# Optimization experiments

Measured on AMD Instinct MI355X. Metric: run time of the kernel, lower is better.

## Reference

```python
import jax, jax.numpy as jnp
import numpy as np
import math

B, S, D, H = 2, 2048, 1024, 16
DH = D // H
PHI = (1 + math.sqrt(5)) / 2

def _carrier_phases(n_heads):
    # DimensionalHeadManager: 7 rungs with weights 1/phi^i, base phases k*pi/7,
    # per-rung heads spread uniformly around the circle.
    base = [k * math.pi / 7 for k in range(7)]
    raw_w = [1.0 / PHI ** i for i in range(7)]
    tw = sum(raw_w)
    alloc = [max(1, round(n_heads * w / tw)) for w in raw_w]
    while sum(alloc) > n_heads:
        alloc[alloc.index(max(alloc))] -= 1
    while sum(alloc) < n_heads:
        alloc[alloc.index(max(alloc))] += 1
    phases = []
    for r, c in enumerate(alloc):
        for j in range(c):
            phases.append(base[r] + 2 * math.pi / max(c, 1) * j)
    return np.array(phases, dtype=np.float32)

def setup_inputs() -> dict:
    key = jax.random.key(0)
    ks = jax.random.split(key, 8)
    x = jax.random.normal(ks[0], (B, S, D), dtype=jnp.float32)
    input_phase = jax.random.uniform(ks[1], (B, S), dtype=jnp.float32) * (2 * math.pi)
    sc = 1.0 / math.sqrt(D)
    Wq = jax.random.normal(ks[2], (D, D), dtype=jnp.float32) * sc
    Wk = jax.random.normal(ks[3], (D, D), dtype=jnp.float32) * sc
    Wv = jax.random.normal(ks[4], (D, D), dtype=jnp.float32) * sc
    Wo = jax.random.normal(ks[5], (D, D), dtype=jnp.float32) * sc
    gamma = jnp.ones((D,), dtype=jnp.float32)
    beta = jnp.zeros((D,), dtype=jnp.float32)
    # per-head fractal compression exponents > 1 (sub-linear for |x|<1)
    exponents = 1.0 + 0.5 * jax.random.uniform(ks[6], (H,), dtype=jnp.float32)
    carrier_phases = jnp.asarray(_carrier_phases(H))
    balance = jnp.asarray(0.5, dtype=jnp.float32)  # BALANCE
    return {"x": x, "input_phase": input_phase, "Wq": Wq, "Wk": Wk, "Wv": Wv,
            "Wo": Wo, "gamma": gamma, "beta": beta, "exponents": exponents,
            "carrier_phases": carrier_phases, "balance": balance}

def _layernorm(x, gamma, beta, eps=1e-5):
    mu = jnp.mean(x, axis=-1, keepdims=True)
    var = jnp.var(x, axis=-1, keepdims=True)
    return (x - mu) * jax.lax.rsqrt(var + eps) * gamma + beta

def _fractal_compress(kv, exps):
    # sign-preserving power-law compression, per-head exponent
    sign = jnp.sign(kv)
    mag = jnp.maximum(jnp.abs(kv), 1e-8)
    return sign * mag ** exps  # exps broadcast (1,H,1,1)

def reference(x, input_phase, Wq, Wk, Wv, Wo, gamma, beta, exponents,
              carrier_phases, balance):
    h = _layernorm(x, gamma, beta)
    def split_heads(t):
        return t.reshape(B, S, H, DH).transpose(0, 2, 1, 3)  # (B,H,S,dh)
    q = split_heads(h @ Wq)
    k = split_heads(h @ Wk)
    v = split_heads(h @ Wv)
    exps = exponents.reshape(1, H, 1, 1)
    k_c = _fractal_compress(k, exps)
    v_c = _fractal_compress(v, exps)
    # per-head carrier resonance: (B,S,H) in [0,1]
    T = jnp.cos((input_phase[:, :, None] - carrier_phases[None, None, :]) / 2.0) ** 2
    Th = T.transpose(0, 2, 1)  # (B,H,S)
    # balance temperature tau = clip(1/(2*balance), 0.1, 10)
    tau = jnp.clip(1.0 / (2.0 * balance + 1e-8), 0.1, 10.0)
    scores = jnp.einsum('bhqd,bhkd->bhqk', q, k_c) / math.sqrt(DH)
    # phase modulation: key-side resonance enters scores in log-space
    scores = scores + jnp.log(Th[:, :, None, :] + 1e-6)
    causal = jnp.tril(jnp.ones((S, S), dtype=bool))
    scores = jnp.where(causal[None, None], scores, jnp.float32(-1e9))
    attn = jax.nn.softmax(scores / tau, axis=-1)
    out = jnp.einsum('bhqk,bhkd->bhqd', attn, v_c)
    # query-side resonance gates the per-head output
    out = out * Th[:, :, :, None]
    out = out.transpose(0, 2, 1, 3).reshape(B, S, D)
    return x + out @ Wo
```

## Files before the change

### kernel.cpp

```cpp
#include <hip/hip_runtime.h>
#include <math.h>

namespace {
constexpr int B = 2, S = 2048, D = 1024, H = 16, DH = 64;
constexpr int BH = B * H;
constexpr int BS = B * S;
constexpr size_t MAT = (size_t)BS * D;
constexpr int QT = S / 64;
}

typedef __attribute__((ext_vector_type(8))) short s16x8;
typedef __attribute__((ext_vector_type(4))) short s16x4;
typedef __attribute__((ext_vector_type(4))) float f32x4;

__device__ inline unsigned short f2bf(float f) {
  union { float f; unsigned u; } c; c.f = f;
  unsigned r = c.u + 0x7fffu + ((c.u >> 16) & 1u);
  return (unsigned short)(r >> 16);
}
__device__ inline short f2bft(float f) {
  union { float f; unsigned u; } c; c.f = f;
  return (short)((c.u + 0x8000u) >> 16);
}
__device__ inline float bf2f(short s) {
  union { unsigned u; float f; } c;
  c.u = ((unsigned)(unsigned short)s) << 16;
  return c.f;
}
__device__ inline void gld16(const unsigned short* g, unsigned short* l) {
  __builtin_amdgcn_global_load_lds(
      (const __attribute__((address_space(1))) unsigned int*)g,
      (__attribute__((address_space(3))) unsigned int*)l, 16, 0, 0);
}

__global__ __launch_bounds__(256) void k_prep(
    const float* __restrict__ x, const float* __restrict__ gamma,
    const float* __restrict__ beta, unsigned short* __restrict__ h,
    const float* __restrict__ phase, const float* __restrict__ cp,
    const float* __restrict__ bal, float* __restrict__ Th,
    float* __restrict__ Lt, const float* __restrict__ W0,
    const float* __restrict__ W1, const float* __restrict__ W2,
    const float* __restrict__ W3, unsigned short* __restrict__ T0,
    unsigned short* __restrict__ T1, unsigned short* __restrict__ T2,
    unsigned short* __restrict__ T3) {
  __shared__ float shbuf[32 * 33];
  int id = blockIdx.x;
  int t = threadIdx.x;
  if (id < 4096) {
    int z = id & 3;
    int bx = ((id >> 2) & 31) * 32;
    int by = (id >> 7) * 32;
    const float* W = (z == 0) ? W0 : (z == 1) ? W1 : (z == 2) ? W2 : W3;
    unsigned short* T = (z == 0) ? T0 : (z == 1) ? T1 : (z == 2) ? T2 : T3;
    int tc = t & 31, tr = t >> 5;
    float(*tile)[33] = (float(*)[33])shbuf;
#pragma unroll
    for (int i = 0; i < 4; i++)
      tile[tr + 8 * i][tc] = W[(size_t)(by + tr + 8 * i) * D + bx + tc];
    __syncthreads();
#pragma unroll
    for (int i = 0; i < 4; i++)
      T[(size_t)(bx + tr + 8 * i) * D + by + tc] = f2bf(tile[tc][tr + 8 * i]);
  } else if (id < 8192) {
    int row = id - 4096;
    float* red = shbuf;
    const float* xr = x + (size_t)row * D;
    float v[4];
    float s = 0.f;
#pragma unroll
    for (int i = 0; i < 4; i++) {
      v[i] = xr[t + 256 * i];
      s += v[i];
    }
    red[t] = s;
    __syncthreads();
    for (int off = 128; off > 0; off >>= 1) {
      if (t < off) red[t] += red[t + off];
      __syncthreads();
    }
    float mu = red[0] * (1.0f / D);
    __syncthreads();
    float s2 = 0.f;
#pragma unroll
    for (int i = 0; i < 4; i++) {
      float d0 = v[i] - mu;
      s2 += d0 * d0;
    }
    red[t] = s2;
    __syncthreads();
    for (int off = 128; off > 0; off >>= 1) {
      if (t < off) red[t] += red[t + off];
      __syncthreads();
    }
    float r = rsqrtf(red[0] * (1.0f / D) + 1e-5f);
    unsigned short* hr = h + (size_t)row * D;
#pragma unroll
    for (int i = 0; i < 4; i++) {
      int c = t + 256 * i;
      hr[c] = f2bf((v[i] - mu) * r * gamma[c] + beta[c]);
    }
  } else {
    int idx = (id - 8192) * 256 + t;
    int s = idx & (S - 1);
    int bh = idx >> 11;
    int hh = bh & (H - 1);
    int b = bh >> 4;
    float tau = fminf(fmaxf(1.0f / (2.0f * bal[0] + 1e-8f), 0.1f), 10.0f);
    float c = cosf((phase[b * S + s] - cp[hh]) * 0.5f);
    float T = c * c;
    Th[idx] = T;
    Lt[idx] = __log2f(T + 1e-6f) * (1.0f / tau);
  }
}

#define MFMA_GEMM_LOOP_TBUF(AP, BP)                                           \
  do {                                                                        \
    gld16(AP, &As[0][chunkA][0]);                                             \
    gld16(AP + (size_t)16 * D, &As[0][chunkA + 16][0]);                       \
    gld16(BP, &Bs[0][chunkA][0]);                                             \
    gld16(BP + (size_t)16 * D, &Bs[0][chunkA + 16][0]);                       \
    gld16(AP + 32, &As[1][chunkA][0]);                                        \
    gld16(AP + (size_t)16 * D + 32, &As[1][chunkA + 16][0]);                  \
    gld16(BP + 32, &Bs[1][chunkA][0]);                                        \
    gld16(BP + (size_t)16 * D + 32, &Bs[1][chunkA + 16][0]);                  \
    int cur = 0;                                                              \
    for (int k0 = 0; k0 < D; k0 += 32) {                                      \
      if (k0 + 32 < D)                                                        \
        asm volatile("s_waitcnt vmcnt(4)" ::: "memory");                      \
      else                                                                    \
        asm volatile("s_waitcnt vmcnt(0)" ::: "memory");                      \
      asm volatile("s_barrier" ::: "memory");                                 \
      if (k0 + 64 < D) {                                                      \
        int nxt = (cur >= 1) ? cur - 1 : 2;                    \
        gld16(AP + k0 + 64, &As[nxt][chunkA][0]);                             \
        gld16(AP + (size_t)16 * D + k0 + 64, &As[nxt][chunkA + 16][0]);       \
        gld16(BP + k0 + 64, &Bs[nxt][chunkA][0]);                             \
        gld16(BP + (size_t)16 * D + k0 + 64, &Bs[nxt][chunkA + 16][0]);       \
      }                                                                       \
      s16x8 af[4], bf[4];                                                     \
      _Pragma("unroll") for (int i = 0; i < 4; i++) {                         \
        af[i] = *(const s16x8*)&As[cur][wm + i * 16 + lane16][quad * 8];      \
        bf[i] = *(const s16x8*)&Bs[cur][wn + i * 16 + lane16][quad * 8];      \
      }                                                                       \
      _Pragma("unroll") for (int i = 0; i < 4; i++)                           \
          _Pragma("unroll") for (int j = 0; j < 4; j++) acc[i][j] =           \
          __builtin_amdgcn_mfma_f32_16x16x32_bf16(af[i], bf[j], acc[i][j],    \
                                                  0, 0, 0);                   \
      cur = (cur == 2) ? 0 : cur + 1;                                         \
    }                                                                         \
  } while (0)

__global__ __launch_bounds__(512) void k_gemm_qkvv(
    const unsigned short* __restrict__ hm, const unsigned short* __restrict__ Wq,
    const unsigned short* __restrict__ Wk, const unsigned short* __restrict__ Wv,
    const float* __restrict__ exps, unsigned short* __restrict__ q,
    unsigned short* __restrict__ kc, unsigned short* __restrict__ vt) {
  __shared__ __align__(16) unsigned short As[3][256][32];
  __shared__ __align__(16) unsigned short Bs[3][128][32];
  int id = blockIdx.x;
  int xcd = id & 7;
  int g = id >> 3;
  int z = g >> 4;
  int w = g & 15;
  const unsigned short *Ap, *Bp;
  int tileM, tileN;
  if (z < 2) {
    Ap = hm; Bp = (z == 0) ? Wq : Wk;
    tileM = ((xcd >> 1) * 4 + (w >> 2)) * 256;
    tileN = ((xcd & 1) * 4 + (w & 3)) * 128;
  } else {
    Ap = Wv; Bp = hm;
    tileM = ((xcd & 1) * 2 + (w >> 3)) * 256;
    tileN = ((xcd >> 1) * 8 + (w & 7)) * 128;
  }
  int t = threadIdx.x;
  int wave = t >> 6, lane = t & 63, lane16 = lane & 15, quad = lane >> 4;
  int wm = (wave >> 1) * 64;
  int wn = (wave & 1) * 64;
  int chunkA = wave * 32;
  int chunkB = wave * 16;
  int srow = (lane >> 2), scol = (lane & 3) * 8;
  const unsigned short* aptr = Ap + (size_t)(tileM + chunkA + srow) * D + scol;
  const unsigned short* bptr = Bp + (size_t)(tileN + chunkB + srow) * D + scol;
  f32x4 acc[4][4] = {};
  gld16(aptr, &As[0][chunkA][0]);
  gld16(aptr + (size_t)16 * D, &As[0][chunkA + 16][0]);
  gld16(bptr, &Bs[0][chunkB][0]);
  gld16(aptr + 32, &As[1][chunkA][0]);
  gld16(aptr + (size_t)16 * D + 32, &As[1][chunkA + 16][0]);
  gld16(bptr + 32, &Bs[1][chunkB][0]);
  int cur = 0;
  for (int k0 = 0; k0 < D; k0 += 32) {
    if (k0 + 32 < D)
      asm volatile("s_waitcnt vmcnt(3)" ::: "memory");
    else
      asm volatile("s_waitcnt vmcnt(0)" ::: "memory");
    asm volatile("s_barrier" ::: "memory");
    if (k0 + 64 < D) {
      int nxt = (cur >= 1) ? cur - 1 : 2;
      gld16(aptr + k0 + 64, &As[nxt][chunkA][0]);
      gld16(aptr + (size_t)16 * D + k0 + 64, &As[nxt][chunkA + 16][0]);
      gld16(bptr + k0 + 64, &Bs[nxt][chunkB][0]);
    }
    s16x8 af[4], bf[4];
#pragma unroll
    for (int i = 0; i < 4; i++) {
      af[i] = *(const s16x8*)&As[cur][wm + i * 16 + lane16][quad * 8];
      bf[i] = *(const s16x8*)&Bs[cur][wn + i * 16 + lane16][quad * 8];
    }
#pragma unroll
    for (int i = 0; i < 4; i++)
#pragma unroll
      for (int j = 0; j < 4; j++)
        acc[i][j] = __builtin_amdgcn_mfma_f32_16x16x32_bf16(af[i], bf[j],
                                                            acc[i][j], 0, 0, 0);
    cur = (cur == 2) ? 0 : cur + 1;
  }
  if (z < 2) {
    unsigned short* __restrict__ outp = (z == 0) ? q : kc;
    float e0 = exps[tileN >> 6];
    float e1 = exps[(tileN >> 6) + 1];
#pragma unroll
    for (int i = 0; i < 4; i++) {
#pragma unroll
      for (int r = 0; r < 4; r++) {
        int row = tileM + wm + i * 16 + quad * 4 + r;
        int b = row >> 11, s = row & (S - 1);
#pragma unroll
        for (int j = 0; j < 4; j++) {
          int cloc = wn + j * 16 + lane16;
          int head = (tileN + cloc) >> 6;
          int dh = cloc & 63;
          float val = acc[i][j][r];
          if (z != 0) {
            float e = (cloc >> 6) ? e1 : e0;
            float sgn = (val > 0.f) ? 1.f : ((val < 0.f) ? -1.f : 0.f);
            float mg = fmaxf(fabsf(val), 1e-8f);
            val = sgn * exp2f(e * __log2f(mg));
          }
          outp[((size_t)(b * H + head) * S + s) * DH + dh] = f2bf(val);
        }
      }
    }
  } else {
#pragma unroll
    for (int i = 0; i < 4; i++) {
#pragma unroll
      for (int r = 0; r < 4; r++) {
        int m = tileM + wm + i * 16 + quad * 4 + r;
        int head = m >> 6, dh = m & 63;
        float e = exps[head];
#pragma unroll
        for (int j = 0; j < 4; j++) {
          int n = tileN + wn + j * 16 + lane16;
          int b = n >> 11, s = n & (S - 1);
          float val = acc[i][j][r];
          float sgn = (val > 0.f) ? 1.f : ((val < 0.f) ? -1.f : 0.f);
          float mg = fmaxf(fabsf(val), 1e-8f);
          val = sgn * exp2f(e * __log2f(mg));
          vt[((size_t)(b * H + head) * DH + dh) * S + s] = f2bf(val);
        }
      }
    }
  }
}

__global__ __launch_bounds__(256) void k_gemm_out_mfma(
    const unsigned short* __restrict__ am, const unsigned short* __restrict__ Wt,
    const float* __restrict__ x, float* __restrict__ outp) {
  __shared__ __align__(16) unsigned short As[3][128][32];
  __shared__ __align__(16) unsigned short Bs[3][128][32];
  int id = blockIdx.x;
  int xcd = id & 7;
  int inner = id >> 3;
  int tileM = ((xcd >> 1) * 8 + (inner >> 2)) * 128;
  int tileN = ((xcd & 1) * 4 + (inner & 3)) * 128;
  int t = threadIdx.x;
  int wave = t >> 6, lane = t & 63, lane16 = lane & 15, quad = lane >> 4;
  int wm = (wave >> 1) * 64, wn = (wave & 1) * 64;
  int chunkA = wave * 32;
  int srow = (lane >> 2), scol = (lane & 3) * 8;
  const unsigned short* aptr = am + (size_t)(tileM + chunkA + srow) * D + scol;
  const unsigned short* bptr = Wt + (size_t)(tileN + chunkA + srow) * D + scol;
  f32x4 acc[4][4] = {};
  MFMA_GEMM_LOOP_TBUF(aptr, bptr);
#pragma unroll
  for (int i = 0; i < 4; i++) {
#pragma unroll
    for (int r = 0; r < 4; r++) {
      int row = tileM + wm + i * 16 + quad * 4 + r;
      const float* xr = x + (size_t)row * D;
      float* orow = outp + (size_t)row * D;
#pragma unroll
      for (int j = 0; j < 4; j++) {
        int col = tileN + wn + j * 16 + lane16;
        orow[col] = xr[col] + acc[i][j][r];
      }
    }
  }
}

__global__ __launch_bounds__(256) void k_attn_mfma(
    const unsigned short* __restrict__ q, const unsigned short* __restrict__ kc,
    const unsigned short* __restrict__ vt, const float* __restrict__ Th,
    const float* __restrict__ Lt, const float* __restrict__ bal,
    unsigned short* __restrict__ ao) {
  __shared__ __align__(16) unsigned short Ks[2][64][72];
  __shared__ __align__(16) unsigned short Vs[2][64][72];
  __shared__ __align__(16) unsigned short Pt[4][16][72];
  __shared__ __align__(16) float Lts[2][64];
  int id = blockIdx.x;
  int bh = (id & 7) + 8 * ((id >> 3) & 3);
  int qt = QT - 1 - (id >> 5);
  int t = threadIdx.x;
  int wave = t >> 6, lane = t & 63;
  int lane16 = lane & 15, quad = lane >> 4;
  float tau = fminf(fmaxf(1.0f / (2.0f * bal[0] + 1e-8f), 0.1f), 10.0f);
  float c1 = 0.125f * (1.0f / tau) * 1.44269504f;
  const unsigned short* qb = q + (size_t)bh * S * DH;
  const unsigned short* kb = kc + (size_t)bh * S * DH;
  const unsigned short* vb = vt + (size_t)bh * DH * S;
  const float* Ltb = Lt + (size_t)bh * S;
  int b = bh >> 4, hh = bh & (H - 1);
  int cr = t >> 3, cc = (t & 7) * 8;
  s16x8 nk0, nk1, nv0, nv1;
  float4 nlt;
#define STAGE_LOAD(KT)                                                  \
  do {                                                                  \
    nk0 = *(const s16x8*)(kb + (size_t)((KT) * 64 + cr) * DH + cc);     \
    nk1 = *(const s16x8*)(kb + (size_t)((KT) * 64 + cr + 32) * DH + cc);\
    nv0 = *(const s16x8*)(vb + (size_t)cr * S + (KT) * 64 + cc);        \
    nv1 = *(const s16x8*)(vb + (size_t)(cr + 32) * S + (KT) * 64 + cc); \
    if (t < 16) nlt = ((const float4*)(Ltb + (KT) * 64))[t];            \
  } while (0)
#define STAGE_WRITE(BF)                                                 \
  do {                                                                  \
    *(s16x8*)&Ks[BF][cr][cc] = nk0;                                     \
    *(s16x8*)&Ks[BF][cr + 32][cc] = nk1;                                \
    *(s16x8*)&Vs[BF][cr][cc] = nv0;                                     \
    *(s16x8*)&Vs[BF][cr + 32][cc] = nv1;                                \
    if (t < 16) ((float4*)Lts[BF])[t] = nlt;                            \
  } while (0)
  int qbase = qt * 64 + wave * 16;
  s16x8 qa0, qa1;
  {
    s16x8 r0 = *(const s16x8*)(qb + (size_t)(qbase + lane16) * DH + quad * 8);
    s16x8 r1 =
        *(const s16x8*)(qb + (size_t)(qbase + lane16) * DH + 32 + quad * 8);
#pragma unroll
    for (int i = 0; i < 8; i++) {
      qa0[i] = f2bft(bf2f(r0[i]) * c1);
      qa1[i] = f2bft(bf2f(r1[i]) * c1);
    }
  }
  STAGE_LOAD(0);
  STAGE_WRITE(0);
  __syncthreads();
  f32x4 O[4] = {};
  float lacc = 0.f;
  for (int kt = 0; kt <= qt; kt++) {
    int cur = kt & 1;
    if (kt < qt) STAGE_LOAD(kt + 1);
    bool diag = (kt == qt);
#pragma unroll
    for (int jk = 0; jk < 4; jk++) {
      s16x8 ka0 = *(const s16x8*)&Ks[cur][jk * 16 + lane16][quad * 8];
      s16x8 ka1 = *(const s16x8*)&Ks[cur][jk * 16 + lane16][32 + quad * 8];
      f32x4 st = {};
      st = __builtin_amdgcn_mfma_f32_16x16x32_bf16(ka0, qa0, st, 0, 0, 0);
      st = __builtin_amdgcn_mfma_f32_16x16x32_bf16(ka1, qa1, st, 0, 0, 0);
      float4 ltv = *(const float4*)&Lts[cur][jk * 16 + quad * 4];
      float lt4[4] = {ltv.x, ltv.y, ltv.z, ltv.w};
      s16x4 pk;
#pragma unroll
      for (int r = 0; r < 4; r++) {
        float vv = fminf(st[r] + lt4[r], 126.f);
        float p = exp2f(vv);
        if (diag)
          p = (jk * 16 + quad * 4 + r <= wave * 16 + lane16) ? p : 0.f;
        lacc += p;
        pk[r] = f2bft(p);
      }
      *(s16x4*)&Pt[wave][lane16][jk * 16 + quad * 4] = pk;
    }
    s16x8 pf0 = *(const s16x8*)&Pt[wave][lane16][quad * 8];
    s16x8 pf1 = *(const s16x8*)&Pt[wave][lane16][32 + quad * 8];
#pragma unroll
    for (int d = 0; d < 4; d++) {
      s16x8 av0 = *(const s16x8*)&Vs[cur][d * 16 + lane16][quad * 8];
      s16x8 av1 = *(const s16x8*)&Vs[cur][d * 16 + lane16][32 + quad * 8];
      O[d] = __builtin_amdgcn_mfma_f32_16x16x32_bf16(av0, pf0, O[d], 0, 0, 0);
      O[d] = __builtin_amdgcn_mfma_f32_16x16x32_bf16(av1, pf1, O[d], 0, 0, 0);
    }
    if (kt < qt) STAGE_WRITE(cur ^ 1);
    __syncthreads();
  }
  lacc += __shfl_xor(lacc, 16, 64);
  lacc += __shfl_xor(lacc, 32, 64);
  int qg = qbase + lane16;
  float scl = Th[(size_t)bh * S + qg] / lacc;
  unsigned short* op = ao + (size_t)(b * S + qg) * D + hh * DH;
#pragma unroll
  for (int d = 0; d < 4; d++) {
    s16x4 pk;
#pragma unroll
    for (int r = 0; r < 4; r++) pk[r] = f2bft(O[d][r] * scl);
    *(s16x4*)(op + d * 16 + quad * 4) = pk;
  }
#undef STAGE_LOAD
#undef STAGE_WRITE
}

extern "C" void kernel_launch(void* const* d_in, const int* in_sizes, int n_in,
                              void* d_out, int out_size, void* d_ws,
                              size_t ws_size, hipStream_t stream) {
  const float* x = (const float*)d_in[0];
  const float* phase = (const float*)d_in[1];
  const float* Wq = (const float*)d_in[2];
  const float* Wk = (const float*)d_in[3];
  const float* Wv = (const float*)d_in[4];
  const float* Wo = (const float*)d_in[5];
  const float* gamma = (const float*)d_in[6];
  const float* beta = (const float*)d_in[7];
  const float* exps = (const float*)d_in[8];
  const float* cph = (const float*)d_in[9];
  const float* bal = (const float*)d_in[10];
  float* out = (float*)d_out;

  unsigned short* hbuf = (unsigned short*)d_ws;
  float* Thbuf = (float*)(hbuf + MAT);
  float* Ltbuf = Thbuf + (size_t)BH * S;
  unsigned short* qbuf = (unsigned short*)(Ltbuf + (size_t)BH * S);
  unsigned short* kbuf = qbuf + MAT;
  unsigned short* vtbuf = kbuf + MAT;
  unsigned short* aobuf = vtbuf + MAT;
  unsigned short* wq_t = aobuf + MAT;
  unsigned short* wk_t = wq_t + (size_t)D * D;
  unsigned short* wv_t = wk_t + (size_t)D * D;
  unsigned short* wo_t = wv_t + (size_t)D * D;

  hipLaunchKernelGGL(k_prep, dim3(8448), dim3(256), 0, stream, x, gamma, beta,
                     hbuf, phase, cph, bal, Thbuf, Ltbuf, Wq, Wk, Wv, Wo, wq_t,
                     wk_t, wv_t, wo_t);
  hipLaunchKernelGGL(k_gemm_qkvv, dim3(384), dim3(512), 0, stream, hbuf, wq_t,
                     wk_t, wv_t, exps, qbuf, kbuf, vtbuf);
  hipLaunchKernelGGL(k_attn_mfma, dim3(1024), dim3(256), 0, stream, qbuf,
                     kbuf, vtbuf, Thbuf, Ltbuf, bal, aobuf);
  hipLaunchKernelGGL(k_gemm_out_mfma, dim3(256), dim3(256), 0, stream, aobuf,
                     wo_t, x, out);
}
```

Baseline: 203.3 us.

## Enlarge attention query tile to 128 rows, two query groups per wave

```diff
diff --git a/kernel.cpp b/kernel.cpp
--- a/kernel.cpp
+++ b/kernel.cpp
@@ -6,7 +6,6 @@
 constexpr int BH = B * H;
 constexpr int BS = B * S;
 constexpr size_t MAT = (size_t)BS * D;
-constexpr int QT = S / 64;
 }
 
 typedef __attribute__((ext_vector_type(8))) short s16x8;
@@ -307,11 +306,11 @@
     unsigned short* __restrict__ ao) {
   __shared__ __align__(16) unsigned short Ks[2][64][72];
   __shared__ __align__(16) unsigned short Vs[2][64][72];
-  __shared__ __align__(16) unsigned short Pt[4][16][72];
+  __shared__ __align__(16) unsigned short Pt[4][32][72];
   __shared__ __align__(16) float Lts[2][64];
   int id = blockIdx.x;
   int bh = (id & 7) + 8 * ((id >> 3) & 3);
-  int qt = QT - 1 - (id >> 5);
+  int qt = 15 - (id >> 5);
   int t = threadIdx.x;
   int wave = t >> 6, lane = t & 63;
   int lane16 = lane & 15, quad = lane >> 4;
@@ -341,71 +340,97 @@
     *(s16x8*)&Vs[BF][cr + 32][cc] = nv1;                                \
     if (t < 16) ((float4*)Lts[BF])[t] = nlt;                            \
   } while (0)
-  int qbase = qt * 64 + wave * 16;
-  s16x8 qa0, qa1;
-  {
-    s16x8 r0 = *(const s16x8*)(qb + (size_t)(qbase + lane16) * DH + quad * 8);
-    s16x8 r1 =
-        *(const s16x8*)(qb + (size_t)(qbase + lane16) * DH + 32 + quad * 8);
+  int qbase = qt * 128 + wave * 32;
+  s16x8 qa[2][2];
+#pragma unroll
+  for (int qg = 0; qg < 2; qg++) {
+    s16x8 r0 = *(const s16x8*)(qb +
+        (size_t)(qbase + qg * 16 + lane16) * DH + quad * 8);
+    s16x8 r1 = *(const s16x8*)(qb +
+        (size_t)(qbase + qg * 16 + lane16) * DH + 32 + quad * 8);
 #pragma unroll
     for (int i = 0; i < 8; i++) {
-      qa0[i] = f2bft(bf2f(r0[i]) * c1);
-      qa1[i] = f2bft(bf2f(r1[i]) * c1);
+      qa[qg][0][i] = f2bft(bf2f(r0[i]) * c1);
+      qa[qg][1][i] = f2bft(bf2f(r1[i]) * c1);
     }
   }
   STAGE_LOAD(0);
   STAGE_WRITE(0);
   __syncthreads();
-  f32x4 O[4] = {};
-  float lacc = 0.f;
-  for (int kt = 0; kt <= qt; kt++) {
+  f32x4 O[2][4] = {};
+  float la[2] = {0.f, 0.f};
+  int ktmax = 2 * qt + 1;
+  for (int kt = 0; kt <= ktmax; kt++) {
     int cur = kt & 1;
-    if (kt < qt) STAGE_LOAD(kt + 1);
-    bool diag = (kt == qt);
-#pragma unroll
-    for (int jk = 0; jk < 4; jk++) {
-      s16x8 ka0 = *(const s16x8*)&Ks[cur][jk * 16 + lane16][quad * 8];
-      s16x8 ka1 = *(const s16x8*)&Ks[cur][jk * 16 + lane16][32 + quad * 8];
-      f32x4 st = {};
-      st = __builtin_amdgcn_mfma_f32_16x16x32_bf16(ka0, qa0, st, 0, 0, 0);
-      st = __builtin_amdgcn_mfma_f32_16x16x32_bf16(ka1, qa1, st, 0, 0, 0);
-      float4 ltv = *(const float4*)&Lts[cur][jk * 16 + quad * 4];
-      float lt4[4] = {ltv.x, ltv.y, ltv.z, ltv.w};
+    if (kt < ktmax) STAGE_LOAD(kt + 1);
+    bool partial = (kt >= 2 * qt);
+#pragma unroll
+    for (int qg = 0; qg < 2; qg++) {
+      int wr = wave * 32 + qg * 16 + lane16;
+#pragma unroll
+      for (int jk = 0; jk < 4; jk++) {
+        s16x8 ka0 = *(const s16x8*)&Ks[cur][jk * 16 + lane16][quad * 8];
+        s16x8 ka1 = *(const s16x8*)&Ks[cur][jk * 16 + lane16][32 + quad * 8];
+        f32x4 st = {};
+        st = __builtin_amdgcn_mfma_f32_16x16x32_bf16(ka0, qa[qg][0], st, 0, 0, 0);
+        st = __builtin_amdgcn_mfma_f32_16x16x32_bf16(ka1, qa[qg][1], st, 0, 0, 0);
+        float4 ltv = *(const float4*)&Lts[cur][jk * 16 + quad * 4];
+        float lt4[4] = {ltv.x, ltv.y, ltv.z, ltv.w};
+        s16x4 pk;
+        if (partial) {
+          int kbase = (kt - 2 * qt) * 64 + jk * 16 + quad * 4;
+#pragma unroll
+          for (int r = 0; r < 4; r++) {
+            float vv = fminf(st[r] + lt4[r], 126.f);
+            float p = exp2f(vv);
+            p = (kbase + r <= wr) ? p : 0.f;
+            la[qg] += p;
+            pk[r] = f2bft(p);
+          }
+        } else {
+#pragma unroll
+          for (int r = 0; r < 4; r++) {
+            float vv = fminf(st[r] + lt4[r], 126.f);
+            float p = exp2f(vv);
+            la[qg] += p;
+            pk[r] = f2bft(p);
+          }
+        }
+        *(s16x4*)&Pt[wave][qg * 16 + lane16][jk * 16 + quad * 4] = pk;
+      }
+    }
+#pragma unroll
+    for (int qg = 0; qg < 2; qg++) {
+      s16x8 pf0 = *(const s16x8*)&Pt[wave][qg * 16 + lane16][quad * 8];
+      s16x8 pf1 = *(const s16x8*)&Pt[wave][qg * 16 + lane16][32 + quad * 8];
+#pragma unroll
+      for (int d = 0; d < 4; d++) {
+        s16x8 av0 = *(const s16x8*)&Vs[cur][d * 16 + lane16][quad * 8];
+        s16x8 av1 = *(const s16x8*)&Vs[cur][d * 16 + lane16][32 + quad * 8];
+        O[qg][d] =
+            __builtin_amdgcn_mfma_f32_16x16x32_bf16(av0, pf0, O[qg][d], 0, 0, 0);
+        O[qg][d] =
+            __builtin_amdgcn_mfma_f32_16x16x32_bf16(av1, pf1, O[qg][d], 0, 0, 0);
+      }
+    }
+    if (kt < ktmax) STAGE_WRITE(cur ^ 1);
+    __syncthreads();
+  }
+#pragma unroll
+  for (int qg = 0; qg < 2; qg++) {
+    float lacc = la[qg];
+    lacc += __shfl_xor(lacc, 16, 64);
+    lacc += __shfl_xor(lacc, 32, 64);
+    int qg_row = qbase + qg * 16 + lane16;
+    float scl = Th[(size_t)bh * S + qg_row] / lacc;
+    unsigned short* op = ao + (size_t)(b * S + qg_row) * D + hh * DH;
+#pragma unroll
+    for (int d = 0; d < 4; d++) {
       s16x4 pk;
 #pragma unroll
-      for (int r = 0; r < 4; r++) {
-        float vv = fminf(st[r] + lt4[r], 126.f);
-        float p = exp2f(vv);
-        if (diag)
-          p = (jk * 16 + quad * 4 + r <= wave * 16 + lane16) ? p : 0.f;
-        lacc += p;
-        pk[r] = f2bft(p);
-      }
-      *(s16x4*)&Pt[wave][lane16][jk * 16 + quad * 4] = pk;
-    }
-    s16x8 pf0 = *(const s16x8*)&Pt[wave][lane16][quad * 8];
-    s16x8 pf1 = *(const s16x8*)&Pt[wave][lane16][32 + quad * 8];
-#pragma unroll
-    for (int d = 0; d < 4; d++) {
-      s16x8 av0 = *(const s16x8*)&Vs[cur][d * 16 + lane16][quad * 8];
-      s16x8 av1 = *(const s16x8*)&Vs[cur][d * 16 + lane16][32 + quad * 8];
-      O[d] = __builtin_amdgcn_mfma_f32_16x16x32_bf16(av0, pf0, O[d], 0, 0, 0);
-      O[d] = __builtin_amdgcn_mfma_f32_16x16x32_bf16(av1, pf1, O[d], 0, 0, 0);
-    }
-    if (kt < qt) STAGE_WRITE(cur ^ 1);
-    __syncthreads();
-  }
-  lacc += __shfl_xor(lacc, 16, 64);
-  lacc += __shfl_xor(lacc, 32, 64);
-  int qg = qbase + lane16;
-  float scl = Th[(size_t)bh * S + qg] / lacc;
-  unsigned short* op = ao + (size_t)(b * S + qg) * D + hh * DH;
-#pragma unroll
-  for (int d = 0; d < 4; d++) {
-    s16x4 pk;
-#pragma unroll
-    for (int r = 0; r < 4; r++) pk[r] = f2bft(O[d][r] * scl);
-    *(s16x4*)(op + d * 16 + quad * 4) = pk;
+      for (int r = 0; r < 4; r++) pk[r] = f2bft(O[qg][d][r] * scl);
+      *(s16x4*)(op + d * 16 + quad * 4) = pk;
+    }
   }
 #undef STAGE_LOAD
 #undef STAGE_WRITE
@@ -444,7 +469,7 @@
                      wk_t, wv_t, wo_t);
   hipLaunchKernelGGL(k_gemm_qkvv, dim3(384), dim3(512), 0, stream, hbuf, wq_t,
                      wk_t, wv_t, exps, qbuf, kbuf, vtbuf);
-  hipLaunchKernelGGL(k_attn_mfma, dim3(1024), dim3(256), 0, stream, qbuf,
+  hipLaunchKernelGGL(k_attn_mfma, dim3(512), dim3(256), 0, stream, qbuf,
                      kbuf, vtbuf, Thbuf, Ltbuf, bal, aobuf);
   hipLaunchKernelGGL(k_gemm_out_mfma, dim3(256), dim3(256), 0, stream, aobuf,
                      wo_t, x, out);
```

Measured after the change: 223.6 us. +10.0%, slower.
